# Performance work log

Measured on AMD Instinct MI355X. Metric: run time of the kernel, lower is better.

The kernel has to match this reference:

```python
import jax, jax.numpy as jnp
import numpy as np

B, N, C, H = 2, 2048, 1024, 16
D = C // H  # head_dim = 64


def _rope_freqs(n, d_half, theta=10000.0):
    inv = 1.0 / (theta ** (np.arange(0, d_half, dtype=np.float32) / d_half))
    ang = np.arange(n, dtype=np.float32)[:, None] * inv[None, :]
    return jnp.asarray(np.cos(ang)), jnp.asarray(np.sin(ang))


def setup_inputs() -> dict:
    key = jax.random.key(0)
    ks = jax.random.split(key, 5)
    cos, sin = _rope_freqs(N, D // 2)
    s = 0.02
    return {
        "x": jax.random.normal(ks[0], (B, N, C), jnp.float32),
        "w_qkv": jax.random.normal(ks[1], (3 * C, C), jnp.float32) * s,
        "b_qkv": jnp.zeros((3 * C,), jnp.float32),
        "w_proj": jax.random.normal(ks[2], (C, C), jnp.float32) * s,
        "b_proj": jnp.zeros((C,), jnp.float32),
        "freqs_cos": cos,
        "freqs_sin": sin,
    }


def _apply_rope(t, cos, sin):
    # t: (B, H, N, D); consecutive pairs (even, odd) form complex numbers,
    # matching torch.view_as_complex on reshape(..., D//2, 2).
    te = t[..., 0::2]
    to = t[..., 1::2]
    cos = cos[None, None, :, :]  # (1,1,N,D//2)
    sin = sin[None, None, :, :]
    oe = te * cos - to * sin
    oo = te * sin + to * cos
    return jnp.stack([oe, oo], axis=-1).reshape(t.shape)


def reference(x, w_qkv, b_qkv, w_proj, b_proj, freqs_cos, freqs_sin):
    b, n, c = x.shape
    qkv = x @ w_qkv.T + b_qkv                      # (B,N,3C)
    qkv = qkv.reshape(b, n, 3, H, D).transpose(2, 0, 3, 1, 4)  # (3,B,H,N,D)
    q, k, v = qkv[0], qkv[1], qkv[2]
    q = _apply_rope(q, freqs_cos, freqs_sin)
    k = _apply_rope(k, freqs_cos, freqs_sin)
    scale = 1.0 / jnp.sqrt(jnp.asarray(D, x.dtype))
    scores = jnp.einsum("bhqd,bhkd->bhqk", q, k) * scale
    attn = jax.nn.softmax(scores, axis=-1)
    out = jnp.einsum("bhqk,bhkd->bhqd", attn, v)   # (B,H,N,D)
    out = out.transpose(0, 2, 1, 3).reshape(b, n, c)
    return out @ w_proj.T + b_proj
```

## Files before the change

kernel.cpp:

```cpp
#include <hip/hip_runtime.h>
#include <hip/hip_bf16.h>
#include <stdint.h>

#define BB 2
#define NN 2048
#define CC 1024
#define HH 16
#define DD 64
#define C3 3072

typedef __attribute__((ext_vector_type(8))) short bf16x8;
typedef __attribute__((ext_vector_type(4))) short bf16x4;
typedef __attribute__((ext_vector_type(4))) float f32x4;
typedef __attribute__((ext_vector_type(16))) float f32x16;
typedef __attribute__((ext_vector_type(4))) unsigned short ushort4_t;

__device__ __forceinline__ unsigned short f2bf(float f) {
  union { float f; unsigned u; } v; v.f = f;
  unsigned r = v.u + 0x7FFFu + ((v.u >> 16) & 1u);
  return (unsigned short)(r >> 16);
}

#if __has_builtin(__builtin_amdgcn_exp2f)
#define EXP2(x) __builtin_amdgcn_exp2f(x)
#else
#define EXP2(x) exp2f(x)
#endif

__device__ __forceinline__ unsigned pack_bf2(float a, float b) {
  union { float f; unsigned u; } ua, ub; ua.f = a; ub.f = b;
#if __has_builtin(__builtin_amdgcn_perm)
  return __builtin_amdgcn_perm(ub.u, ua.u, 0x07060302u);
#else
  return (ua.u >> 16) | (ub.u & 0xFFFF0000u);
#endif
}

#define QSCALE 0.18033688f

#define GLDS(g, l) __builtin_amdgcn_global_load_lds( \
    (const __attribute__((address_space(1))) void*)(g), \
    (__attribute__((address_space(3))) void*)(l), 16, 0, 0)

__global__ __launch_bounds__(256) void k_cvt(
    const float* __restrict__ x, const float* __restrict__ wq,
    const float* __restrict__ wp,
    unsigned short* __restrict__ xb, unsigned short* __restrict__ wqb,
    unsigned short* __restrict__ wpb)
{
  int blk = blockIdx.x;
  const float* s; unsigned short* d; int i;
  if (blk < 4096)      { s = x;  d = xb;  i = blk * 256 + threadIdx.x; }
  else if (blk < 7168) { s = wq; d = wqb; i = (blk - 4096) * 256 + threadIdx.x; }
  else                 { s = wp; d = wpb; i = (blk - 7168) * 256 + threadIdx.x; }
  float4 v = ((const float4*)s)[i];
  ushort4_t o;
  o.x = f2bf(v.x); o.y = f2bf(v.y); o.z = f2bf(v.z); o.w = f2bf(v.w);
  ((ushort4_t*)d)[i] = o;
}

__global__ __launch_bounds__(256) void k_gemm_qkv(
    const unsigned short* __restrict__ A, const unsigned short* __restrict__ Bt,
    const float* __restrict__ bias,
    const float* __restrict__ cosb, const float* __restrict__ sinb,
    unsigned short* __restrict__ Qg, unsigned short* __restrict__ Kg,
    unsigned short* __restrict__ Vt)
{
  __shared__ __align__(16) unsigned short Sh[16384];
  const int tid  = threadIdx.x;
  const int lane = tid & 63;
  const int wave = tid >> 6;
  const int bm = blockIdx.y * 128;
  const int bn = blockIdx.x * 128;
  const int wm = (wave >> 1) * 64;
  const int wn = (wave & 1) * 64;
  const int frow = lane & 15;
  const int fks  = (((lane >> 4) ^ ((frow >> 1) & 3)) * 8);
  const int K = 1024;
  const int NIT = K / 32;

  f32x4 acc[4][4] = {};

  const int row0 = tid >> 2, cc0 = tid & 3;
  const int row1 = row0 + 64;
  const int scc = (cc0 ^ ((row0 >> 1) & 3)) * 8;
  const unsigned short* Arow0 = A  + (size_t)(bm + row0) * K + scc;
  const unsigned short* Arow1 = A  + (size_t)(bm + row1) * K + scc;
  const unsigned short* Brow0 = Bt + (size_t)(bn + row0) * K + scc;
  const unsigned short* Brow1 = Bt + (size_t)(bn + row1) * K + scc;

  GLDS(Arow0, Sh + (size_t)tid * 8);
  GLDS(Brow0, Sh + 4096 + (size_t)tid * 8);
  GLDS(Arow1, Sh + (size_t)(tid + 256) * 8);
  GLDS(Brow1, Sh + 4096 + (size_t)(tid + 256) * 8);

  for (int it = 0; it < NIT; ++it) {
    const int p = it & 1;
    const unsigned short* As = Sh + p * 8192;
    const unsigned short* Bs = As + 4096;
    __syncthreads();

    if (it + 1 < NIT) {
      const int k1 = (it + 1) * 32;
      unsigned short* An = Sh + (1 - p) * 8192;
      GLDS(Arow0 + k1, An + (size_t)tid * 8);
      GLDS(Brow0 + k1, An + 4096 + (size_t)tid * 8);
      GLDS(Arow1 + k1, An + (size_t)(tid + 256) * 8);
      GLDS(Brow1 + k1, An + 4096 + (size_t)(tid + 256) * 8);
    }

    bf16x8 af[4], bfr[4];
#pragma unroll
    for (int t = 0; t < 4; ++t) {
      af[t]  = *(const bf16x8*)(As + (wm + t * 16 + frow) * 32 + fks);
      bfr[t] = *(const bf16x8*)(Bs + (wn + t * 16 + frow) * 32 + fks);
    }
#pragma unroll
    for (int mt = 0; mt < 4; ++mt)
#pragma unroll
      for (int nt = 0; nt < 4; ++nt)
        acc[mt][nt] = __builtin_amdgcn_mfma_f32_16x16x32_bf16(af[mt], bfr[nt], acc[mt][nt], 0, 0, 0);
  }
  __syncthreads();

  const int er0  = (lane >> 4) * 4;
  const int ecol = lane & 15;
  const int region = bn >> 10;
  const int gcol0 = bn + wn;
  const int h  = (gcol0 >> 6) & 15;
  const int rowg0 = bm + wm;
  const int b  = rowg0 >> 11;
  const int n0 = rowg0 & (NN - 1);
  unsigned short* wt = Sh + wave * 4096;

#pragma unroll
  for (int nt = 0; nt < 4; ++nt) {
    const int c64 = nt * 16 + ecol;
    const float bv = bias[gcol0 + c64];
    const int ii  = c64 >> 1;
#pragma unroll
    for (int mt = 0; mt < 4; ++mt)
#pragma unroll
      for (int r = 0; r < 4; ++r) {
        const int ml = mt * 16 + er0 + r;
        const int n  = n0 + ml;
        float v = acc[mt][nt][r] + bv;
        float vp = __shfl_xor(v, 1, 64);
        if (region == 2) {
          wt[c64 * 64 + ((((ml >> 3) ^ (c64 & 7)) << 3) | (ml & 7))] = f2bf(v);
        } else {
          float cth = cosb[n * 32 + ii], sth = sinb[n * 32 + ii];
          float ov = (c64 & 1) ? (vp * sth + v * cth)
                               : (v * cth - vp * sth);
          if (region == 0) ov *= QSCALE;
          wt[ml * 64 + ((((c64 >> 3) ^ (ml & 7)) << 3) | (c64 & 7))] = f2bf(ov);
        }
      }
  }

  const int rr = lane >> 3, cc = lane & 7;
  if (region == 2) {
    unsigned short* dst = Vt + (size_t)(b * HH + h) * DD * NN + n0;
    const int q8a = (cc >> 1) * 2;
    const int q8b = q8a + 1;
    const int half = (cc & 1) * 4;
#pragma unroll
    for (int it = 0; it < 8; ++it) {
      int dl = it * 8 + rr;
      union { bf16x4 h[2]; bf16x8 w; } vv;
      vv.h[0] = *(const bf16x4*)(wt + dl * 64 + ((q8a ^ (dl & 7)) << 3) + half);
      vv.h[1] = *(const bf16x4*)(wt + dl * 64 + ((q8b ^ (dl & 7)) << 3) + half);
      *(bf16x8*)(dst + (size_t)dl * NN + cc * 8) = vv.w;
    }
  } else {
    unsigned short* dqk = ((region == 0) ? Qg : Kg) +
                          ((size_t)(b * HH + h) * NN + n0) * DD;
#pragma unroll
    for (int it = 0; it < 8; ++it) {
      int ml = it * 8 + rr;
      bf16x8 vv = *(const bf16x8*)(wt + ml * 64 + ((cc ^ (ml & 7)) << 3));
      *(bf16x8*)(dqk + (size_t)ml * DD + cc * 8) = vv;
    }
  }
}

__global__ __launch_bounds__(512) void k_attn(
    const unsigned short* __restrict__ Qg, const unsigned short* __restrict__ Kg,
    const unsigned short* __restrict__ Vtg, unsigned short* __restrict__ Og)
{
  __shared__ __align__(16) unsigned short Ks[4][64 * 64];
  __shared__ __align__(16) unsigned short Vs[4][64 * 64];

  const int tid  = threadIdx.x;
  const int lane = tid & 63;
  const int wave = tid >> 6;
  const int wid  = (blockIdx.x & 7) * 32 + (blockIdx.x >> 3);
  const int bh = wid >> 3;
  const int qt = wid & 7;
  const int q0 = qt * 256 + wave * 32;
  const int l31 = lane & 31;
  const int hi  = lane >> 5;
  const int s7  = l31 & 7;

  const unsigned short* Qb = Qg  + (size_t)bh * NN * DD;
  const unsigned short* Kb = Kg  + (size_t)bh * NN * DD;
  const unsigned short* Vb = Vtg + (size_t)bh * DD * NN;

  int soffB[4];
#pragma unroll
  for (int i = 0; i < 4; ++i)
    soffB[i] = (l31 * 64 + (((2 * i + hi) ^ s7) << 3)) * 2;

  bf16x8 qf[4];
#pragma unroll
  for (int dc = 0; dc < 4; ++dc)
    qf[dc] = *(const bf16x8*)(Qb + (size_t)(q0 + l31) * DD + dc * 16 + hi * 8);

  bf16x8 ones;
#pragma unroll
  for (int i = 0; i < 8; ++i) ones[i] = (short)0x3F80;
  const f32x16 zero16 = {};

  f32x16 oacc[2] = {};
  f32x16 lacc = {};

  const int row0 = tid >> 3, cc0 = tid & 7;
  const int sw0 = (cc0 ^ (row0 & 7)) * 8;

#define STAGE64(bf, j) do { \
    GLDS(Kb + (size_t)((j) + row0) * DD + sw0, Ks[bf] + (size_t)tid * 8); \
    GLDS(Vb + (size_t)row0 * NN + (j) + sw0,   Vs[bf] + (size_t)tid * 8); \
  } while (0)

  STAGE64(0, 0);
  STAGE64(1, 64);

  const int NT = NN / 128;
#pragma unroll 2
  for (int t = 0; t < NT; ++t) {
    const int p = t & 1;
    __syncthreads();

    if (t + 1 < NT) {
      STAGE64(2 * (1 - p),     (t + 1) * 128);
      STAGE64(2 * (1 - p) + 1, (t + 1) * 128 + 64);
    }

#pragma unroll
    for (int sub = 0; sub < 2; ++sub) {
      const char* KsB = (const char*)Ks[2 * p + sub];
      const char* VsB = (const char*)Vs[2 * p + sub];

      f32x16 sacc[2];
      __builtin_amdgcn_s_setprio(1);
#pragma unroll
      for (int T = 0; T < 2; ++T) {
        bf16x8 kf0 = *(const bf16x8*)(KsB + T * 4096 + soffB[0]);
        sacc[T] = __builtin_amdgcn_mfma_f32_32x32x16_bf16(kf0, qf[0], zero16, 0, 0, 0);
#pragma unroll
        for (int dc = 1; dc < 4; ++dc) {
          bf16x8 kf = *(const bf16x8*)(KsB + T * 4096 + soffB[dc]);
          sacc[T] = __builtin_amdgcn_mfma_f32_32x32x16_bf16(kf, qf[dc], sacc[T], 0, 0, 0);
        }
      }
      __builtin_amdgcn_s_setprio(0);

#pragma unroll
      for (int T = 0; T < 2; ++T) {
        unsigned pk[8];
#pragma unroll
        for (int jj = 0; jj < 8; ++jj) {
          float e0 = EXP2(sacc[T][2 * jj]);
          float e1 = EXP2(sacc[T][2 * jj + 1]);
          pk[jj] = pack_bf2(e0, e1);
        }
        union { unsigned u[4]; bf16x8 v; } fa, fb;
        fa.u[0] = pk[0]; fa.u[1] = pk[1]; fa.u[2] = pk[2]; fa.u[3] = pk[3];
        fb.u[0] = pk[4]; fb.u[1] = pk[5]; fb.u[2] = pk[6]; fb.u[3] = pk[7];
        __builtin_amdgcn_s_setprio(1);
#pragma unroll
        for (int dt = 0; dt < 2; ++dt) {
          bf16x8 v0 = *(const bf16x8*)(VsB + dt * 4096 + soffB[2 * T + 0]);
          bf16x8 v1 = *(const bf16x8*)(VsB + dt * 4096 + soffB[2 * T + 1]);
          oacc[dt] = __builtin_amdgcn_mfma_f32_32x32x16_bf16(fa.v, v0, oacc[dt], 0, 0, 0);
          oacc[dt] = __builtin_amdgcn_mfma_f32_32x32x16_bf16(fb.v, v1, oacc[dt], 0, 0, 0);
        }
        lacc = __builtin_amdgcn_mfma_f32_32x32x16_bf16(fa.v, ones, lacc, 0, 0, 0);
        lacc = __builtin_amdgcn_mfma_f32_32x32x16_bf16(fb.v, ones, lacc, 0, 0, 0);
        __builtin_amdgcn_s_setprio(0);
      }
    }
  }
#undef STAGE64

  const int b = bh >> 4;
  const int h = bh & 15;
#pragma unroll
  for (int r = 0; r < 16; ++r) {
    const int qr = (r & 3) + 8 * (r >> 2) + 4 * hi;
    const float linv = 1.0f / lacc[r];
    unsigned short* orow = Og + (size_t)(b * NN + q0 + qr) * CC + h * DD + l31;
    orow[0]  = f2bf(oacc[0][r] * linv);
    orow[32] = f2bf(oacc[1][r] * linv);
  }
}

__global__ __launch_bounds__(256) void k_gemm_proj(
    const unsigned short* __restrict__ A, const unsigned short* __restrict__ Bt,
    const float* __restrict__ bias, float* __restrict__ Co)
{
  __shared__ __align__(16) unsigned short As[4][64 * 32];
  __shared__ __align__(16) unsigned short Bs[4][128 * 32];
  const int tid  = threadIdx.x;
  const int lane = tid & 63;
  const int wave = tid >> 6;
  const int bm = blockIdx.y * 64;
  const int bn = blockIdx.x * 128;
  const int wm = (wave >> 1) * 32;
  const int wn = (wave & 1) * 64;
  const int frow = lane & 15;
  const int fks  = (((lane >> 4) ^ ((frow >> 1) & 3)) * 8);
  const int K = 1024;

  f32x4 acc[2][4] = {};

  const int row0 = tid >> 2, cc0 = tid & 3;
  const int scc = (cc0 ^ ((row0 >> 1) & 3)) * 8;
  const unsigned short* Arow  = A  + (size_t)(bm + row0) * K + scc;
  const unsigned short* Brow0 = Bt + (size_t)(bn + row0) * K + scc;
  const unsigned short* Brow1 = Bt + (size_t)(bn + row0 + 64) * K + scc;

#define STAGEP(bf, k1) do { \
    GLDS(Arow  + (k1), As[bf] + (size_t)tid * 8); \
    GLDS(Brow0 + (k1), Bs[bf] + (size_t)tid * 8); \
    GLDS(Brow1 + (k1), Bs[bf] + (size_t)(tid + 256) * 8); \
  } while (0)

  STAGEP(0, 0);
  STAGEP(1, 32);

  const int NT = K / 64;
  for (int t = 0; t < NT; ++t) {
    const int p = t & 1;
    __syncthreads();

    if (t + 1 < NT) {
      STAGEP(2 * (1 - p),     (t + 1) * 64);
      STAGEP(2 * (1 - p) + 1, (t + 1) * 64 + 32);
    }

#pragma unroll
    for (int sub = 0; sub < 2; ++sub) {
      const unsigned short* Asb = As[2 * p + sub];
      const unsigned short* Bsb = Bs[2 * p + sub];
      bf16x8 af[2], bfr[4];
#pragma unroll
      for (int q = 0; q < 2; ++q)
        af[q] = *(const bf16x8*)(Asb + (wm + q * 16 + frow) * 32 + fks);
#pragma unroll
      for (int q = 0; q < 4; ++q)
        bfr[q] = *(const bf16x8*)(Bsb + (wn + q * 16 + frow) * 32 + fks);
#pragma unroll
      for (int mt = 0; mt < 2; ++mt)
#pragma unroll
        for (int nt = 0; nt < 4; ++nt)
          acc[mt][nt] = __builtin_amdgcn_mfma_f32_16x16x32_bf16(af[mt], bfr[nt], acc[mt][nt], 0, 0, 0);
    }
  }
#undef STAGEP

  const int er0  = (lane >> 4) * 4;
  const int ecol = lane & 15;
#pragma unroll
  for (int nt = 0; nt < 4; ++nt) {
    int col = bn + wn + nt * 16 + ecol;
    float bv = bias[col];
#pragma unroll
    for (int mt = 0; mt < 2; ++mt)
#pragma unroll
      for (int r = 0; r < 4; ++r) {
        int rowg = bm + wm + mt * 16 + er0 + r;
        Co[(size_t)rowg * CC + col] = acc[mt][nt][r] + bv;
      }
  }
}

extern "C" void kernel_launch(void* const* d_in, const int* in_sizes, int n_in,
                              void* d_out, int out_size, void* d_ws, size_t ws_size,
                              hipStream_t stream)
{
  const float* x      = (const float*)d_in[0];
  const float* w_qkv  = (const float*)d_in[1];
  const float* b_qkv  = (const float*)d_in[2];
  const float* w_proj = (const float*)d_in[3];
  const float* b_proj = (const float*)d_in[4];
  const float* fcos   = (const float*)d_in[5];
  const float* fsin   = (const float*)d_in[6];
  float* out = (float*)d_out;

  char* ws = (char*)d_ws;
  unsigned short* xb     = (unsigned short*)(ws);
  unsigned short* wqkvb  = (unsigned short*)(ws + 8388608);
  unsigned short* wprojb = (unsigned short*)(ws + 14680064);
  unsigned short* Qb     = (unsigned short*)(ws + 16777216);
  unsigned short* Kb     = (unsigned short*)(ws + 25165824);
  unsigned short* Vtb    = (unsigned short*)(ws + 33554432);
  unsigned short* aob    = (unsigned short*)(ws + 41943040);

  k_cvt<<<8192, 256, 0, stream>>>(x, w_qkv, w_proj, xb, wqkvb, wprojb);

  k_gemm_qkv<<<dim3(24, 32), 256, 0, stream>>>(xb, wqkvb, b_qkv, fcos, fsin,
                                               Qb, Kb, Vtb);

  k_attn<<<256, 512, 0, stream>>>(Qb, Kb, Vtb, aob);

  k_gemm_proj<<<dim3(8, 64), 256, 0, stream>>>(aob, wprojb, b_proj, out);
}
```

Baseline: 191.4 us.

## Triple-buffer QKV GEMM shared-memory staging with explicit vmcnt waits

The QKV projection GEMM moves from double-buffered to triple-buffered global-to-LDS staging, prefetching two K-tiles ahead. The per-iteration __syncthreads is replaced by a partial s_waitcnt vmcnt plus s_barrier, so one tile's loads can still be in flight during compute. The aim is to hide more global load latency behind the MFMAs. In exchange, LDS use grows from 32 KB to 48 KB per block, which may reduce occupancy, and correctness now depends on the hand-set vmcnt counts.

```diff
diff --git a/kernel.cpp b/kernel.cpp
--- a/kernel.cpp
+++ b/kernel.cpp
@@ -66,7 +66,7 @@
     unsigned short* __restrict__ Qg, unsigned short* __restrict__ Kg,
     unsigned short* __restrict__ Vt)
 {
-  __shared__ __align__(16) unsigned short Sh[16384];
+  __shared__ __align__(16) unsigned short Sh[24576];
   const int tid  = threadIdx.x;
   const int lane = tid & 63;
   const int wave = tid >> 6;
@@ -89,25 +89,28 @@
   const unsigned short* Brow0 = Bt + (size_t)(bn + row0) * K + scc;
   const unsigned short* Brow1 = Bt + (size_t)(bn + row1) * K + scc;
 
-  GLDS(Arow0, Sh + (size_t)tid * 8);
-  GLDS(Brow0, Sh + 4096 + (size_t)tid * 8);
-  GLDS(Arow1, Sh + (size_t)(tid + 256) * 8);
-  GLDS(Brow1, Sh + 4096 + (size_t)(tid + 256) * 8);
-
+#define STAGEQ(bf, k1) do { \
+    unsigned short* An = Sh + (bf) * 8192; \
+    GLDS(Arow0 + (k1), An + (size_t)tid * 8); \
+    GLDS(Brow0 + (k1), An + 4096 + (size_t)tid * 8); \
+    GLDS(Arow1 + (k1), An + (size_t)(tid + 256) * 8); \
+    GLDS(Brow1 + (k1), An + 4096 + (size_t)(tid + 256) * 8); \
+  } while (0)
+
+  STAGEQ(0, 0);
+  STAGEQ(1, 32);
+
+  int bc = 0;
+  int bs = 2;
   for (int it = 0; it < NIT; ++it) {
-    const int p = it & 1;
-    const unsigned short* As = Sh + p * 8192;
+    if (it == NIT - 1) asm volatile("s_waitcnt vmcnt(0)" ::: "memory");
+    else               asm volatile("s_waitcnt vmcnt(4)" ::: "memory");
+    __builtin_amdgcn_s_barrier();
+
+    if (it + 2 < NIT) STAGEQ(bs, (it + 2) * 32);
+
+    const unsigned short* As = Sh + bc * 8192;
     const unsigned short* Bs = As + 4096;
-    __syncthreads();
-
-    if (it + 1 < NIT) {
-      const int k1 = (it + 1) * 32;
-      unsigned short* An = Sh + (1 - p) * 8192;
-      GLDS(Arow0 + k1, An + (size_t)tid * 8);
-      GLDS(Brow0 + k1, An + 4096 + (size_t)tid * 8);
-      GLDS(Arow1 + k1, An + (size_t)(tid + 256) * 8);
-      GLDS(Brow1 + k1, An + 4096 + (size_t)(tid + 256) * 8);
-    }
 
     bf16x8 af[4], bfr[4];
 #pragma unroll
@@ -120,7 +123,11 @@
 #pragma unroll
       for (int nt = 0; nt < 4; ++nt)
         acc[mt][nt] = __builtin_amdgcn_mfma_f32_16x16x32_bf16(af[mt], bfr[nt], acc[mt][nt], 0, 0, 0);
-  }
+
+    bc = (bc == 2) ? 0 : bc + 1;
+    bs = (bs == 2) ? 0 : bs + 1;
+  }
+#undef STAGEQ
   __syncthreads();
 
   const int er0  = (lane >> 4) * 4;
```

Result: slower. 206.5 us (+7.9%).
